# Kernel tuning notes

Measured on AMD Instinct MI355X. Metric: run time of the kernel, lower is better.

Reference implementation:

```python
import jax, jax.numpy as jnp
import numpy as np

B, C, H, W = 8, 512, 32, 32
NUM_HEADS = 8
NUM_GROUPS = 32
EPS = 1e-5


def setup_inputs() -> dict:
    key = jax.random.key(0)
    ks = jax.random.split(key, 7)
    x = jax.random.normal(ks[0], (B, C, H, W), dtype=jnp.float32)
    # GroupNorm affine params
    gamma = jnp.ones((C,), dtype=jnp.float32)
    beta = jnp.zeros((C,), dtype=jnp.float32)
    # qkv 1x1 conv1d: weight [3C, C], bias [3C]
    w_qkv = jax.random.normal(ks[1], (3 * C, C), dtype=jnp.float32) * (1.0 / np.sqrt(C))
    b_qkv = jax.random.normal(ks[2], (3 * C,), dtype=jnp.float32) * 0.01
    # proj_out 1x1 conv1d (zero-init in the original; random here so the op is non-trivial)
    w_proj = jax.random.normal(ks[3], (C, C), dtype=jnp.float32) * (1.0 / np.sqrt(C))
    b_proj = jax.random.normal(ks[4], (C,), dtype=jnp.float32) * 0.01
    return {"x": x, "gamma": gamma, "beta": beta, "w_qkv": w_qkv, "b_qkv": b_qkv,
            "w_proj": w_proj, "b_proj": b_proj}


def _group_norm(x, gamma, beta):
    # x: [B, C, L]
    b, c, l = x.shape
    xg = x.reshape(b, NUM_GROUPS, (c // NUM_GROUPS) * l)
    mean = jnp.mean(xg, axis=-1, keepdims=True)
    var = jnp.var(xg, axis=-1, keepdims=True)
    xn = ((xg - mean) * jax.lax.rsqrt(var + EPS)).reshape(b, c, l)
    return xn * gamma[None, :, None] + beta[None, :, None]


def reference(x, gamma, beta, w_qkv, b_qkv, w_proj, b_proj):
    b, c, h, w = x.shape
    L = h * w
    xf = x.reshape(b, c, L)
    xn = _group_norm(xf, gamma, beta)
    # 1x1 conv1d == channel matmul: [B, 3C, L]
    qkv = jnp.einsum('oc,bcl->bol', w_qkv, xn) + b_qkv[None, :, None]
    ch = c // NUM_HEADS  # per-head channels
    q, k, v = jnp.split(qkv, 3, axis=1)
    bh = b * NUM_HEADS
    q = q.reshape(bh, ch, L)
    k = k.reshape(bh, ch, L)
    v = v.reshape(bh, ch, L)
    scale = 1.0 / np.sqrt(np.sqrt(ch))
    weight = jnp.einsum('bct,bcs->bts', q * scale, k * scale)  # [BH, L, L]
    weight = jax.nn.softmax(weight.astype(jnp.float32), axis=-1).astype(q.dtype)
    a = jnp.einsum('bts,bcs->bct', weight, v)  # [BH, ch, L]
    hid = a.reshape(b, c, L)
    hid = jnp.einsum('oc,bcl->bol', w_proj, hid) + b_proj[None, :, None]
    return (xf + hid).reshape(b, c, h, w)
```

## Files before the change

kernel.cpp:

```cpp
#include <hip/hip_runtime.h>

typedef unsigned short u16;
using bf16x8 = __attribute__((ext_vector_type(8))) __bf16;
using f32x4  = __attribute__((ext_vector_type(4))) float;
using f32x16 = __attribute__((ext_vector_type(16))) float;
using u16x8  = __attribute__((ext_vector_type(8))) u16;
using u32x2  = __attribute__((ext_vector_type(2))) unsigned;

constexpr float QSC = 0.180336880111112f;

#define TID ((int)threadIdx.x)

__device__ __forceinline__ float fexp2(float x) {
#if __has_builtin(__builtin_amdgcn_exp2f)
  return __builtin_amdgcn_exp2f(x);
#else
  return exp2f(x);
#endif
}
__device__ __forceinline__ u16 f2bf(float f) {
  __bf16 h = (__bf16)f;
  return __builtin_bit_cast(u16, h);
}
__device__ __forceinline__ unsigned cvtpk(float a, float b) {
  unsigned r;
  asm("v_cvt_pk_bf16_f32 %0, %1, %2" : "=v"(r) : "v"(a), "v"(b));
  return r;
}
__device__ __forceinline__ u32x2 plswap(unsigned d, unsigned s) {
#if __has_builtin(__builtin_amdgcn_permlane32_swap)
  return __builtin_amdgcn_permlane32_swap(d, s, false, false);
#else
  unsigned dx = (unsigned)__shfl_xor((int)d, 32);
  unsigned sx = (unsigned)__shfl_xor((int)s, 32);
  int hh = ((int)threadIdx.x >> 5) & 1;
  u32x2 r;
  r[0] = hh ? d : sx;
  r[1] = hh ? dx : s;
  return r;
#endif
}
__device__ __forceinline__ float xhalf_max(float x) {
  unsigned u = __builtin_bit_cast(unsigned, x);
  u32x2 r = plswap(u, u);
  return fmaxf(__builtin_bit_cast(float, r[0]), __builtin_bit_cast(float, r[1]));
}
__device__ __forceinline__ float xhalf_add(float x) {
  unsigned u = __builtin_bit_cast(unsigned, x);
  u32x2 r = plswap(u, u);
  return __builtin_bit_cast(float, r[0]) + __builtin_bit_cast(float, r[1]);
}
__device__ __forceinline__ bf16x8 ldfrag(const u16* p) {
  return __builtin_bit_cast(bf16x8, *(const u16x8*)p);
}
__device__ __forceinline__ int swz(int row, int ch) {
  return ch ^ (row & 7) ^ ((row >> 3) & 7);
}
__device__ __forceinline__ void gload16(const u16* g, u16* l) {
  __builtin_amdgcn_global_load_lds(
      (__attribute__((address_space(1))) void*)g,
      (__attribute__((address_space(3))) void*)l, 16, 0, 0);
}
__device__ __forceinline__ f32x4 mfma16(bf16x8 a, bf16x8 b, f32x4 c) {
  return __builtin_amdgcn_mfma_f32_16x16x32_bf16(a, b, c, 0, 0, 0);
}
__device__ __forceinline__ f32x16 mfma32(bf16x8 a, bf16x8 b, f32x16 c) {
  return __builtin_amdgcn_mfma_f32_32x32x16_bf16(a, b, c, 0, 0, 0);
}

__global__ __launch_bounds__(256) void prep_stats(
    const float* __restrict__ wq, const float* __restrict__ wp,
    u16* __restrict__ wqb, u16* __restrict__ wpb,
    const float* __restrict__ x, float* __restrict__ stats) {
  __shared__ float sm[4], ssm[4];
  int bid = blockIdx.x;
  if (bid < 1024) {
    int i = bid * 256 + TID;
    if (i < 196608) {
      float4 v = ((const float4*)wq)[i];
      u16* o = wqb + i * 4;
      o[0] = f2bf(v.x); o[1] = f2bf(v.y); o[2] = f2bf(v.z); o[3] = f2bf(v.w);
    } else {
      int j = i - 196608;
      float4 v = ((const float4*)wp)[j];
      u16* o = wpb + j * 4;
      o[0] = f2bf(v.x); o[1] = f2bf(v.y); o[2] = f2bf(v.z); o[3] = f2bf(v.w);
    }
    return;
  }
  int blk = bid - 1024;
  size_t base = ((size_t)blk) << 14;
  const float4* xp = (const float4*)(x + base);
  float s = 0.f, ss = 0.f;
#pragma unroll
  for (int i = 0; i < 16; ++i) {
    float4 v = xp[TID + i * 256];
    s += v.x + v.y + v.z + v.w;
    ss += v.x * v.x + v.y * v.y + v.z * v.z + v.w * v.w;
  }
#pragma unroll
  for (int off = 32; off; off >>= 1) {
    s += __shfl_down(s, off);
    ss += __shfl_down(ss, off);
  }
  if ((TID & 63) == 0) { sm[TID >> 6] = s; ssm[TID >> 6] = ss; }
  __syncthreads();
  if (TID == 0) {
    float tot = sm[0] + sm[1] + sm[2] + sm[3];
    float tots = ssm[0] + ssm[1] + ssm[2] + ssm[3];
    float mean = tot * (1.f / 16384.f);
    float var = tots * (1.f / 16384.f) - mean * mean;
    stats[blk * 2] = mean;
    stats[blk * 2 + 1] = rsqrtf(var + 1e-5f);
  }
}

__global__ __launch_bounds__(256) void gn_apply(
    const float* __restrict__ x, const float* __restrict__ gamma,
    const float* __restrict__ beta, const float* __restrict__ stats,
    u16* __restrict__ xnT) {
  __shared__ u16 xt[32 * 520];
  int l0 = blockIdx.x * 32, b = blockIdx.y;
  int li = TID & 31, cb = TID >> 5;
#pragma unroll 4
  for (int it = 0; it < 64; ++it) {
    int c = it * 8 + cb;
    int g = c >> 4;
    float mean = stats[(b * 32 + g) * 2];
    float rstd = stats[(b * 32 + g) * 2 + 1];
    float ga = gamma[c] * rstd;
    float be = beta[c] - mean * ga;
    float v = x[((size_t)b * 512 + c) * 1024 + l0 + li];
    xt[li * 520 + c] = f2bf(v * ga + be);
  }
  __syncthreads();
  int li2 = TID >> 3, u0 = TID & 7;
#pragma unroll
  for (int it = 0; it < 8; ++it) {
    int unit = u0 + it * 8;
    u16x8 v = *(const u16x8*)&xt[li2 * 520 + unit * 8];
    *(u16x8*)&xnT[((size_t)b * 1024 + l0 + li2) * 512 + unit * 8] = v;
  }
}

__global__ __launch_bounds__(256) void qkv_gemm(
    const u16* __restrict__ A, const u16* __restrict__ Bt,
    const float* __restrict__ bias,
    u16* __restrict__ qT, u16* __restrict__ kT, u16* __restrict__ vbuf) {
  __shared__ u16 Al[8192], Bl[8192];
  int lin = blockIdx.x;
  int b = lin & 7;
  int rem = lin >> 3;
  int mi = rem % 12, ni = rem / 12;
  int m0 = mi * 128, n0 = ni * 128;
  int lane = TID & 63, w = TID >> 6;
  int mw = (w >> 1) * 64, nw = (w & 1) * 64;
  const u16* Bb = Bt + (size_t)b * 1024 * 512;
  f32x4 acc[4][4] = {};
  for (int k0 = 0; k0 < 512; k0 += 64) {
#pragma unroll
    for (int u = 0; u < 4; ++u) {
      int unit = u * 256 + TID, row = unit >> 3, ch = unit & 7;
      gload16(&A[(size_t)(m0 + row) * 512 + k0 + swz(row, ch) * 8], &Al[unit * 8]);
      gload16(&Bb[(size_t)(n0 + row) * 512 + k0 + swz(row, ch) * 8], &Bl[unit * 8]);
    }
    __syncthreads();
    bf16x8 xf[4][2];
#pragma unroll
    for (int xi = 0; xi < 4; ++xi)
#pragma unroll
      for (int kf = 0; kf < 2; ++kf) {
        int row = nw + xi * 16 + (lane & 15);
        int lc = kf * 4 + (lane >> 4);
        xf[xi][kf] = ldfrag(&Bl[row * 64 + swz(row, lc) * 8]);
      }
#pragma unroll
    for (int yi = 0; yi < 4; ++yi) {
      int row = mw + yi * 16 + (lane & 15);
      int lc = lane >> 4;
      bf16x8 y0 = ldfrag(&Al[row * 64 + swz(row, lc) * 8]);
      bf16x8 y1 = ldfrag(&Al[row * 64 + swz(row, lc + 4) * 8]);
#pragma unroll
      for (int xi = 0; xi < 4; ++xi) {
        acc[xi][yi] = mfma16(xf[xi][0], y0, acc[xi][yi]);
        acc[xi][yi] = mfma16(xf[xi][1], y1, acc[xi][yi]);
      }
    }
    __syncthreads();
  }
  int sel = m0 >> 9;
  int ho = w >> 1;
  u16* RP = ho ? Bl : Al;
  if (sel < 2) {
#pragma unroll
    for (int xi = 0; xi < 4; ++xi)
#pragma unroll
      for (int yi = 0; yi < 4; ++yi)
#pragma unroll
        for (int r = 0; r < 4; ++r) {
          int lloc = nw + xi * 16 + (lane >> 4) * 4 + r;
          int oc = yi * 16 + (lane & 15);
          float v = acc[xi][yi][r] + bias[m0 + ho * 64 + oc];
          if (sel == 0) v *= QSC;
          RP[lloc * 64 + swz(lloc, oc >> 3) * 8 + (oc & 7)] = f2bf(v);
        }
    __syncthreads();
    u16* dst = sel ? kT : qT;
    int h0 = (m0 & 511) >> 6;
#pragma unroll
    for (int uu = 0; uu < 4; ++uu) {
      int unit = uu * 256 + TID, row = unit >> 3, ch = unit & 7;
      u16x8 v0 = *(const u16x8*)&Al[row * 64 + swz(row, ch) * 8];
      u16x8 v1 = *(const u16x8*)&Bl[row * 64 + swz(row, ch) * 8];
      *(u16x8*)&dst[((size_t)(b * 8 + h0) * 1024 + n0 + row) * 64 + ch * 8] = v0;
      *(u16x8*)&dst[((size_t)(b * 8 + h0 + 1) * 1024 + n0 + row) * 64 + ch * 8] = v1;
    }
  } else {
#pragma unroll
    for (int xi = 0; xi < 4; ++xi)
#pragma unroll
      for (int yi = 0; yi < 4; ++yi)
#pragma unroll
        for (int r = 0; r < 4; ++r) {
          int lloc = nw + xi * 16 + (lane >> 4) * 4 + r;
          int oc = yi * 16 + (lane & 15);
          float v = acc[xi][yi][r] + bias[m0 + ho * 64 + oc];
          RP[oc * 128 + swz(oc, lloc >> 3) * 8 + (lloc & 7)] = f2bf(v);
        }
    __syncthreads();
    int h0 = (m0 - 1024) >> 6;
#pragma unroll
    for (int uu = 0; uu < 4; ++uu) {
      int unit = uu * 256 + TID, ro = unit >> 4, ch = unit & 15;
      u16x8 v0 = *(const u16x8*)&Al[ro * 128 + swz(ro, ch) * 8];
      u16x8 v1 = *(const u16x8*)&Bl[ro * 128 + swz(ro, ch) * 8];
      *(u16x8*)&vbuf[((size_t)(b * 8 + h0) * 64 + ro) * 1024 + n0 + ch * 8] = v0;
      *(u16x8*)&vbuf[((size_t)(b * 8 + h0 + 1) * 64 + ro) * 1024 + n0 + ch * 8] = v1;
    }
  }
}

__global__ __launch_bounds__(256) void attn_mfma(const u16* __restrict__ qT,
                                                 const u16* __restrict__ kT,
                                                 const u16* __restrict__ vb,
                                                 u16* __restrict__ aT) {
  __shared__ u16 smem[16384];
  int lin = blockIdx.x;
  int rem = lin >> 3;
  int bh = (lin & 7) * 8 + (rem >> 3);
  int t0 = (rem & 7) * 128;
  int b = bh >> 3, hd = bh & 7;
  int lane = TID & 63, w = TID >> 6;
  int h = lane >> 5, ln = lane & 31;
  int t = t0 + w * 32 + ln;
  const u16* qp = qT + ((size_t)bh * 1024 + t) * 64;
  const u16* kbase = kT + (size_t)bh * 1024 * 64;
  const u16* vbase = vb + (size_t)bh * 64 * 1024;
  bf16x8 qf[4];
#pragma unroll
  for (int kc = 0; kc < 4; ++kc) qf[kc] = ldfrag(qp + kc * 16 + h * 8);
  float m_r = -1e30f, l_r = 0.f;
  f32x16 oacc[2] = {};

  int u0 = TID, u1 = TID + 256;
  int r0 = u0 >> 3, c0 = u0 & 7;
  int r1 = u1 >> 3, c1 = u1 & 7;
  {
    u16* Ks = smem;
    u16* Vs = smem + 4096;
    gload16(&kbase[(size_t)r0 * 64 + swz(r0, c0) * 8], &Ks[u0 * 8]);
    gload16(&kbase[(size_t)r1 * 64 + swz(r1, c1) * 8], &Ks[u1 * 8]);
    gload16(&vbase[(size_t)r0 * 1024 + swz(r0, c0) * 8], &Vs[u0 * 8]);
    gload16(&vbase[(size_t)r1 * 1024 + swz(r1, c1) * 8], &Vs[u1 * 8]);
  }
  __syncthreads();
  for (int tile = 0; tile < 16; ++tile) {
    const u16* Ks = smem + (tile & 1) * 8192;
    const u16* Vs = Ks + 4096;
    if (tile < 15) {
      int sn = (tile + 1) * 64;
      u16* Kn = smem + ((tile + 1) & 1) * 8192;
      u16* Vn = Kn + 4096;
      gload16(&kbase[(size_t)(sn + r0) * 64 + swz(r0, c0) * 8], &Kn[u0 * 8]);
      gload16(&kbase[(size_t)(sn + r1) * 64 + swz(r1, c1) * 8], &Kn[u1 * 8]);
      gload16(&vbase[(size_t)r0 * 1024 + sn + swz(r0, c0) * 8], &Vn[u0 * 8]);
      gload16(&vbase[(size_t)r1 * 1024 + sn + swz(r1, c1) * 8], &Vn[u1 * 8]);
    }
    f32x16 sacc[2] = {};
    __builtin_amdgcn_s_setprio(1);
#pragma unroll
    for (int sb = 0; sb < 2; ++sb) {
      int srow = sb * 32 + ln;
#pragma unroll
      for (int kc = 0; kc < 4; ++kc) {
        bf16x8 kf = ldfrag(&Ks[srow * 64 + swz(srow, kc * 2 + h) * 8]);
        sacc[sb] = mfma32(kf, qf[kc], sacc[sb]);
      }
    }
    __builtin_amdgcn_s_setprio(0);
    float mp[4];
#pragma unroll
    for (int q = 0; q < 4; ++q) {
      mp[q] = fmaxf(fmaxf(sacc[0][q * 4], sacc[0][q * 4 + 1]),
                    fmaxf(sacc[0][q * 4 + 2], sacc[0][q * 4 + 3]));
      mp[q] = fmaxf(mp[q], fmaxf(fmaxf(sacc[1][q * 4], sacc[1][q * 4 + 1]),
                                 fmaxf(sacc[1][q * 4 + 2], sacc[1][q * 4 + 3])));
    }
    float mx = xhalf_max(fmaxf(fmaxf(mp[0], mp[1]), fmaxf(mp[2], mp[3])));
    bool noresc = (__all(mx <= m_r + 8.f) != 0);
    if (!noresc) {
      float mn = fmaxf(m_r, mx);
      float al = fexp2(m_r - mn);
      m_r = mn;
      l_r *= al;
#pragma unroll
      for (int ca = 0; ca < 2; ++ca)
#pragma unroll
        for (int i = 0; i < 16; ++i) oacc[ca][i] *= al;
    }
    float rp[4] = {0.f, 0.f, 0.f, 0.f};
#pragma unroll
    for (int sb = 0; sb < 2; ++sb)
#pragma unroll
      for (int i = 0; i < 16; ++i) {
        float pv = fexp2(sacc[sb][i] - m_r);
        sacc[sb][i] = pv;
        rp[i & 3] += pv;
      }
    l_r += xhalf_add((rp[0] + rp[1]) + (rp[2] + rp[3]));
    unsigned W[2][4][2];
#pragma unroll
    for (int sb = 0; sb < 2; ++sb)
#pragma unroll
      for (int p4 = 0; p4 < 4; ++p4)
#pragma unroll
        for (int e = 0; e < 2; ++e)
          W[sb][p4][e] = cvtpk(sacc[sb][p4 * 4 + 2 * e], sacc[sb][p4 * 4 + 2 * e + 1]);
#pragma unroll
    for (int m = 0; m < 4; ++m) {
      int sb = m >> 1, q = (m & 1) * 2;
      unsigned a0 = W[sb][q][0], a1 = W[sb][q][1];
      unsigned b0 = W[sb][q + 1][0], b1 = W[sb][q + 1][1];
      unsigned s0w = h ? a0 : b0;
      unsigned s1w = h ? a1 : b1;
      unsigned x0 = (unsigned)__shfl_xor((int)s0w, 32);
      unsigned x1 = (unsigned)__shfl_xor((int)s1w, 32);
      unsigned w0 = h ? x0 : a0;
      unsigned w1 = h ? x1 : a1;
      unsigned w2 = h ? b0 : x0;
      unsigned w3 = h ? b1 : x1;
      uint4 pw = make_uint4(w0, w1, w2, w3);
      bf16x8 pf = __builtin_bit_cast(bf16x8, pw);
      __builtin_amdgcn_s_setprio(1);
#pragma unroll
      for (int ca = 0; ca < 2; ++ca) {
        int crow = ca * 32 + ln;
        bf16x8 vf = ldfrag(&Vs[crow * 64 + swz(crow, m * 2 + h) * 8]);
        oacc[ca] = mfma32(vf, pf, oacc[ca]);
      }
      __builtin_amdgcn_s_setprio(0);
    }
    __syncthreads();
  }
  float rl = 1.f / l_r;
  int tloc = w * 32 + ln;
#pragma unroll
  for (int ca = 0; ca < 2; ++ca)
#pragma unroll
    for (int p4 = 0; p4 < 4; ++p4)
#pragma unroll
      for (int e = 0; e < 2; ++e) {
        int r = p4 * 4 + e * 2;
        int c = ca * 32 + 8 * p4 + 4 * h + 2 * e;
        unsigned pk = cvtpk(oacc[ca][r] * rl, oacc[ca][r + 1] * rl);
        *(unsigned*)&smem[tloc * 64 + swz(tloc, c >> 3) * 8 + (c & 7)] = pk;
      }
  __syncthreads();
#pragma unroll
  for (int u = 0; u < 4; ++u) {
    int unit = u * 256 + TID;
    int row = unit >> 3, ch = unit & 7;
    u16x8 v = *(const u16x8*)&smem[row * 64 + swz(row, ch) * 8];
    *(u16x8*)&aT[((size_t)b * 1024 + t0 + row) * 512 + hd * 64 + ch * 8] = v;
  }
}

__global__ __launch_bounds__(256) void proj_gemm(
    const u16* __restrict__ A, const u16* __restrict__ Bt,
    const float* __restrict__ bias, const float* __restrict__ resid,
    float* __restrict__ of) {
  __shared__ u16 Al[8192], Bl[8192];
  int lin = blockIdx.x;
  int b = lin & 7;
  int rem = lin >> 3;
  int mi = rem & 3, ni = rem >> 2;
  int m0 = mi * 128, n0 = ni * 128;
  int lane = TID & 63, w = TID >> 6;
  int mw = (w >> 1) * 64, nw = (w & 1) * 64;
  const u16* Bb = Bt + (size_t)b * 1024 * 512;
  f32x4 acc[4][4] = {};
  for (int k0 = 0; k0 < 512; k0 += 64) {
#pragma unroll
    for (int u = 0; u < 4; ++u) {
      int unit = u * 256 + TID, row = unit >> 3, ch = unit & 7;
      gload16(&A[(size_t)(m0 + row) * 512 + k0 + swz(row, ch) * 8], &Al[unit * 8]);
      gload16(&Bb[(size_t)(n0 + row) * 512 + k0 + swz(row, ch) * 8], &Bl[unit * 8]);
    }
    __syncthreads();
    bf16x8 xf[4][2];
#pragma unroll
    for (int xi = 0; xi < 4; ++xi)
#pragma unroll
      for (int kf = 0; kf < 2; ++kf) {
        int row = mw + xi * 16 + (lane & 15);
        int lc = kf * 4 + (lane >> 4);
        xf[xi][kf] = ldfrag(&Al[row * 64 + swz(row, lc) * 8]);
      }
#pragma unroll
    for (int yi = 0; yi < 4; ++yi) {
      int row = nw + yi * 16 + (lane & 15);
      int lc = lane >> 4;
      bf16x8 y0 = ldfrag(&Bl[row * 64 + swz(row, lc) * 8]);
      bf16x8 y1 = ldfrag(&Bl[row * 64 + swz(row, lc + 4) * 8]);
#pragma unroll
      for (int xi = 0; xi < 4; ++xi) {
        acc[xi][yi] = mfma16(xf[xi][0], y0, acc[xi][yi]);
        acc[xi][yi] = mfma16(xf[xi][1], y1, acc[xi][yi]);
      }
    }
    __syncthreads();
  }
#pragma unroll
  for (int xi = 0; xi < 4; ++xi)
#pragma unroll
    for (int yi = 0; yi < 4; ++yi)
#pragma unroll
      for (int r = 0; r < 4; ++r) {
        int o = m0 + mw + xi * 16 + (lane >> 4) * 4 + r;
        int l = n0 + nw + yi * 16 + (lane & 15);
        size_t idx = ((size_t)b * 512 + o) * 1024 + l;
        of[idx] = acc[xi][yi][r] + bias[o] + resid[idx];
      }
}

extern "C" void kernel_launch(void* const* d_in, const int* in_sizes, int n_in,
                              void* d_out, int out_size, void* d_ws, size_t ws_size,
                              hipStream_t stream) {
  const float* x = (const float*)d_in[0];
  const float* gamma = (const float*)d_in[1];
  const float* beta = (const float*)d_in[2];
  const float* w_qkv = (const float*)d_in[3];
  const float* b_qkv = (const float*)d_in[4];
  const float* w_proj = (const float*)d_in[5];
  const float* b_proj = (const float*)d_in[6];
  float* out = (float*)d_out;

  u16* qT = (u16*)d_ws;
  u16* kT = qT + 4194304;
  u16* vbuf = kT + 4194304;
  u16* aTb = vbuf + 4194304;
  u16* wqb = aTb + 4194304;
  u16* wpb = wqb + 786432;
  float* stats = (float*)(wpb + 262144);
  u16* xnT = (u16*)d_out;

  prep_stats<<<dim3(1280), dim3(256), 0, stream>>>(w_qkv, w_proj, wqb, wpb, x, stats);
  gn_apply<<<dim3(32, 8), dim3(256), 0, stream>>>(x, gamma, beta, stats, xnT);
  qkv_gemm<<<dim3(768), dim3(256), 0, stream>>>(wqb, xnT, b_qkv, qT, kT, vbuf);
  attn_mfma<<<dim3(512), dim3(256), 0, stream>>>(qT, kT, vbuf, aTb);
  proj_gemm<<<dim3(256), dim3(256), 0, stream>>>(wpb, aTb, b_proj, x, out);
}
```

Before: 87.34 us.

## Double KV stage size in attention and halve proj GEMM N-tile

The attention kernel now stages 128 keys and values per shared-memory buffer instead of 64, so it runs 8 outer iterations with two 64-wide sub-steps each. This halves the number of barriers and prefetch rounds, at the cost of doubling LDS to 64KB, which may lower occupancy. The projection GEMM uses 128x64 tiles with each wave computing a 32x64 slice, doubling the grid to 512 blocks to fill more CUs. This trades per-block data reuse for more parallelism.

Result: slower. 89.49 us (+2.5%).

```diff
diff --git a/kernel.cpp b/kernel.cpp
--- a/kernel.cpp
+++ b/kernel.cpp
@@ -244,7 +244,7 @@
                                                  const u16* __restrict__ kT,
                                                  const u16* __restrict__ vb,
                                                  u16* __restrict__ aT) {
-  __shared__ u16 smem[16384];
+  __shared__ u16 smem[32768];
   int lin = blockIdx.x;
   int rem = lin >> 3;
   int bh = (lin & 7) * 8 + (rem >> 3);
@@ -262,103 +262,121 @@
   float m_r = -1e30f, l_r = 0.f;
   f32x16 oacc[2] = {};
 
-  int u0 = TID, u1 = TID + 256;
-  int r0 = u0 >> 3, c0 = u0 & 7;
-  int r1 = u1 >> 3, c1 = u1 & 7;
   {
-    u16* Ks = smem;
-    u16* Vs = smem + 4096;
-    gload16(&kbase[(size_t)r0 * 64 + swz(r0, c0) * 8], &Ks[u0 * 8]);
-    gload16(&kbase[(size_t)r1 * 64 + swz(r1, c1) * 8], &Ks[u1 * 8]);
-    gload16(&vbase[(size_t)r0 * 1024 + swz(r0, c0) * 8], &Vs[u0 * 8]);
-    gload16(&vbase[(size_t)r1 * 1024 + swz(r1, c1) * 8], &Vs[u1 * 8]);
+    u16* Kb = smem;
+    u16* Vb = smem + 8192;
+#pragma unroll
+    for (int it = 0; it < 4; ++it) {
+      int unit = it * 256 + TID, row = unit >> 3, ch = unit & 7;
+      gload16(&kbase[(size_t)row * 64 + swz(row, ch) * 8], &Kb[unit * 8]);
+    }
+#pragma unroll
+    for (int it = 0; it < 4; ++it) {
+      int unit = it * 256 + TID;
+      int half = unit >> 9, c = (unit >> 3) & 63, ch = unit & 7;
+      gload16(&vbase[(size_t)c * 1024 + half * 64 + swz(c, ch) * 8], &Vb[unit * 8]);
+    }
   }
   __syncthreads();
-  for (int tile = 0; tile < 16; ++tile) {
-    const u16* Ks = smem + (tile & 1) * 8192;
-    const u16* Vs = Ks + 4096;
-    if (tile < 15) {
-      int sn = (tile + 1) * 64;
-      u16* Kn = smem + ((tile + 1) & 1) * 8192;
-      u16* Vn = Kn + 4096;
-      gload16(&kbase[(size_t)(sn + r0) * 64 + swz(r0, c0) * 8], &Kn[u0 * 8]);
-      gload16(&kbase[(size_t)(sn + r1) * 64 + swz(r1, c1) * 8], &Kn[u1 * 8]);
-      gload16(&vbase[(size_t)r0 * 1024 + sn + swz(r0, c0) * 8], &Vn[u0 * 8]);
-      gload16(&vbase[(size_t)r1 * 1024 + sn + swz(r1, c1) * 8], &Vn[u1 * 8]);
-    }
-    f32x16 sacc[2] = {};
-    __builtin_amdgcn_s_setprio(1);
-#pragma unroll
-    for (int sb = 0; sb < 2; ++sb) {
-      int srow = sb * 32 + ln;
-#pragma unroll
-      for (int kc = 0; kc < 4; ++kc) {
-        bf16x8 kf = ldfrag(&Ks[srow * 64 + swz(srow, kc * 2 + h) * 8]);
-        sacc[sb] = mfma32(kf, qf[kc], sacc[sb]);
-      }
-    }
-    __builtin_amdgcn_s_setprio(0);
-    float mp[4];
-#pragma unroll
-    for (int q = 0; q < 4; ++q) {
-      mp[q] = fmaxf(fmaxf(sacc[0][q * 4], sacc[0][q * 4 + 1]),
-                    fmaxf(sacc[0][q * 4 + 2], sacc[0][q * 4 + 3]));
-      mp[q] = fmaxf(mp[q], fmaxf(fmaxf(sacc[1][q * 4], sacc[1][q * 4 + 1]),
-                                 fmaxf(sacc[1][q * 4 + 2], sacc[1][q * 4 + 3])));
-    }
-    float mx = xhalf_max(fmaxf(fmaxf(mp[0], mp[1]), fmaxf(mp[2], mp[3])));
-    bool noresc = (__all(mx <= m_r + 8.f) != 0);
-    if (!noresc) {
-      float mn = fmaxf(m_r, mx);
-      float al = fexp2(m_r - mn);
-      m_r = mn;
-      l_r *= al;
-#pragma unroll
-      for (int ca = 0; ca < 2; ++ca)
-#pragma unroll
-        for (int i = 0; i < 16; ++i) oacc[ca][i] *= al;
-    }
-    float rp[4] = {0.f, 0.f, 0.f, 0.f};
-#pragma unroll
-    for (int sb = 0; sb < 2; ++sb)
-#pragma unroll
-      for (int i = 0; i < 16; ++i) {
-        float pv = fexp2(sacc[sb][i] - m_r);
-        sacc[sb][i] = pv;
-        rp[i & 3] += pv;
-      }
-    l_r += xhalf_add((rp[0] + rp[1]) + (rp[2] + rp[3]));
-    unsigned W[2][4][2];
-#pragma unroll
-    for (int sb = 0; sb < 2; ++sb)
-#pragma unroll
-      for (int p4 = 0; p4 < 4; ++p4)
-#pragma unroll
-        for (int e = 0; e < 2; ++e)
-          W[sb][p4][e] = cvtpk(sacc[sb][p4 * 4 + 2 * e], sacc[sb][p4 * 4 + 2 * e + 1]);
-#pragma unroll
-    for (int m = 0; m < 4; ++m) {
-      int sb = m >> 1, q = (m & 1) * 2;
-      unsigned a0 = W[sb][q][0], a1 = W[sb][q][1];
-      unsigned b0 = W[sb][q + 1][0], b1 = W[sb][q + 1][1];
-      unsigned s0w = h ? a0 : b0;
-      unsigned s1w = h ? a1 : b1;
-      unsigned x0 = (unsigned)__shfl_xor((int)s0w, 32);
-      unsigned x1 = (unsigned)__shfl_xor((int)s1w, 32);
-      unsigned w0 = h ? x0 : a0;
-      unsigned w1 = h ? x1 : a1;
-      unsigned w2 = h ? b0 : x0;
-      unsigned w3 = h ? b1 : x1;
-      uint4 pw = make_uint4(w0, w1, w2, w3);
-      bf16x8 pf = __builtin_bit_cast(bf16x8, pw);
+  for (int tile = 0; tile < 8; ++tile) {
+    const u16* Kb = smem + (tile & 1) * 16384;
+    const u16* Vb = Kb + 8192;
+    if (tile < 7) {
+      int sn = (tile + 1) * 128;
+      u16* Kn = smem + ((tile + 1) & 1) * 16384;
+      u16* Vn = Kn + 8192;
+#pragma unroll
+      for (int it = 0; it < 4; ++it) {
+        int unit = it * 256 + TID, row = unit >> 3, ch = unit & 7;
+        gload16(&kbase[(size_t)(sn + row) * 64 + swz(row, ch) * 8], &Kn[unit * 8]);
+      }
+#pragma unroll
+      for (int it = 0; it < 4; ++it) {
+        int unit = it * 256 + TID;
+        int half = unit >> 9, c = (unit >> 3) & 63, ch = unit & 7;
+        gload16(&vbase[(size_t)c * 1024 + sn + half * 64 + swz(c, ch) * 8],
+                &Vn[unit * 8]);
+      }
+    }
+#pragma unroll
+    for (int sub = 0; sub < 2; ++sub) {
+      const u16* Ks = Kb + sub * 4096;
+      const u16* Vs = Vb + sub * 4096;
+      f32x16 sacc[2] = {};
       __builtin_amdgcn_s_setprio(1);
 #pragma unroll
-      for (int ca = 0; ca < 2; ++ca) {
-        int crow = ca * 32 + ln;
-        bf16x8 vf = ldfrag(&Vs[crow * 64 + swz(crow, m * 2 + h) * 8]);
-        oacc[ca] = mfma32(vf, pf, oacc[ca]);
+      for (int sb = 0; sb < 2; ++sb) {
+        int srow = sb * 32 + ln;
+#pragma unroll
+        for (int kc = 0; kc < 4; ++kc) {
+          bf16x8 kf = ldfrag(&Ks[srow * 64 + swz(srow, kc * 2 + h) * 8]);
+          sacc[sb] = mfma32(kf, qf[kc], sacc[sb]);
+        }
       }
       __builtin_amdgcn_s_setprio(0);
+      float mp[4];
+#pragma unroll
+      for (int q = 0; q < 4; ++q) {
+        mp[q] = fmaxf(fmaxf(sacc[0][q * 4], sacc[0][q * 4 + 1]),
+                      fmaxf(sacc[0][q * 4 + 2], sacc[0][q * 4 + 3]));
+        mp[q] = fmaxf(mp[q], fmaxf(fmaxf(sacc[1][q * 4], sacc[1][q * 4 + 1]),
+                                   fmaxf(sacc[1][q * 4 + 2], sacc[1][q * 4 + 3])));
+      }
+      float mx = xhalf_max(fmaxf(fmaxf(mp[0], mp[1]), fmaxf(mp[2], mp[3])));
+      bool noresc = (__all(mx <= m_r + 8.f) != 0);
+      if (!noresc) {
+        float mn = fmaxf(m_r, mx);
+        float al = fexp2(m_r - mn);
+        m_r = mn;
+        l_r *= al;
+#pragma unroll
+        for (int ca = 0; ca < 2; ++ca)
+#pragma unroll
+          for (int i = 0; i < 16; ++i) oacc[ca][i] *= al;
+      }
+      float rp[4] = {0.f, 0.f, 0.f, 0.f};
+#pragma unroll
+      for (int sb = 0; sb < 2; ++sb)
+#pragma unroll
+        for (int i = 0; i < 16; ++i) {
+          float pv = fexp2(sacc[sb][i] - m_r);
+          sacc[sb][i] = pv;
+          rp[i & 3] += pv;
+        }
+      l_r += xhalf_add((rp[0] + rp[1]) + (rp[2] + rp[3]));
+      unsigned W[2][4][2];
+#pragma unroll
+      for (int sb = 0; sb < 2; ++sb)
+#pragma unroll
+        for (int p4 = 0; p4 < 4; ++p4)
+#pragma unroll
+          for (int e = 0; e < 2; ++e)
+            W[sb][p4][e] =
+                cvtpk(sacc[sb][p4 * 4 + 2 * e], sacc[sb][p4 * 4 + 2 * e + 1]);
+#pragma unroll
+      for (int m = 0; m < 4; ++m) {
+        int sb = m >> 1, q = (m & 1) * 2;
+        unsigned a0 = W[sb][q][0], a1 = W[sb][q][1];
+        unsigned b0 = W[sb][q + 1][0], b1 = W[sb][q + 1][1];
+        unsigned s0w = h ? a0 : b0;
+        unsigned s1w = h ? a1 : b1;
+        unsigned x0 = (unsigned)__shfl_xor((int)s0w, 32);
+        unsigned x1 = (unsigned)__shfl_xor((int)s1w, 32);
+        unsigned w0 = h ? x0 : a0;
+        unsigned w1 = h ? x1 : a1;
+        unsigned w2 = h ? b0 : x0;
+        unsigned w3 = h ? b1 : x1;
+        uint4 pw = make_uint4(w0, w1, w2, w3);
+        bf16x8 pf = __builtin_bit_cast(bf16x8, pw);
+        __builtin_amdgcn_s_setprio(1);
+#pragma unroll
+        for (int ca = 0; ca < 2; ++ca) {
+          int crow = ca * 32 + ln;
+          bf16x8 vf = ldfrag(&Vs[crow * 64 + swz(crow, m * 2 + h) * 8]);
+          oacc[ca] = mfma32(vf, pf, oacc[ca]);
+        }
+        __builtin_amdgcn_s_setprio(0);
+      }
     }
     __syncthreads();
   }
@@ -389,41 +407,45 @@
     const u16* __restrict__ A, const u16* __restrict__ Bt,
     const float* __restrict__ bias, const float* __restrict__ resid,
     float* __restrict__ of) {
-  __shared__ u16 Al[8192], Bl[8192];
+  __shared__ u16 Al[8192], Bl[4096];
   int lin = blockIdx.x;
   int b = lin & 7;
   int rem = lin >> 3;
-  int mi = rem & 3, ni = rem >> 2;
-  int m0 = mi * 128, n0 = ni * 128;
+  int mi = rem & 3, ni4 = rem >> 2;
+  int m0 = mi * 128, n0 = ni4 * 64;
   int lane = TID & 63, w = TID >> 6;
-  int mw = (w >> 1) * 64, nw = (w & 1) * 64;
+  int mw2 = w * 32;
   const u16* Bb = Bt + (size_t)b * 1024 * 512;
-  f32x4 acc[4][4] = {};
+  f32x4 acc[2][4] = {};
   for (int k0 = 0; k0 < 512; k0 += 64) {
 #pragma unroll
     for (int u = 0; u < 4; ++u) {
       int unit = u * 256 + TID, row = unit >> 3, ch = unit & 7;
       gload16(&A[(size_t)(m0 + row) * 512 + k0 + swz(row, ch) * 8], &Al[unit * 8]);
+    }
+#pragma unroll
+    for (int u = 0; u < 2; ++u) {
+      int unit = u * 256 + TID, row = unit >> 3, ch = unit & 7;
       gload16(&Bb[(size_t)(n0 + row) * 512 + k0 + swz(row, ch) * 8], &Bl[unit * 8]);
     }
     __syncthreads();
-    bf16x8 xf[4][2];
-#pragma unroll
-    for (int xi = 0; xi < 4; ++xi)
+    bf16x8 xf[2][2];
+#pragma unroll
+    for (int xi = 0; xi < 2; ++xi)
 #pragma unroll
       for (int kf = 0; kf < 2; ++kf) {
-        int row = mw + xi * 16 + (lane & 15);
+        int row = mw2 + xi * 16 + (lane & 15);
         int lc = kf * 4 + (lane >> 4);
         xf[xi][kf] = ldfrag(&Al[row * 64 + swz(row, lc) * 8]);
       }
 #pragma unroll
     for (int yi = 0; yi < 4; ++yi) {
-      int row = nw + yi * 16 + (lane & 15);
+      int row = yi * 16 + (lane & 15);
       int lc = lane >> 4;
       bf16x8 y0 = ldfrag(&Bl[row * 64 + swz(row, lc) * 8]);
       bf16x8 y1 = ldfrag(&Bl[row * 64 + swz(row, lc + 4) * 8]);
 #pragma unroll
-      for (int xi = 0; xi < 4; ++xi) {
+      for (int xi = 0; xi < 2; ++xi) {
         acc[xi][yi] = mfma16(xf[xi][0], y0, acc[xi][yi]);
         acc[xi][yi] = mfma16(xf[xi][1], y1, acc[xi][yi]);
       }
@@ -431,13 +453,13 @@
     __syncthreads();
   }
 #pragma unroll
-  for (int xi = 0; xi < 4; ++xi)
+  for (int xi = 0; xi < 2; ++xi)
 #pragma unroll
     for (int yi = 0; yi < 4; ++yi)
 #pragma unroll
       for (int r = 0; r < 4; ++r) {
-        int o = m0 + mw + xi * 16 + (lane >> 4) * 4 + r;
-        int l = n0 + nw + yi * 16 + (lane & 15);
+        int o = m0 + mw2 + xi * 16 + (lane >> 4) * 4 + r;
+        int l = n0 + yi * 16 + (lane & 15);
         size_t idx = ((size_t)b * 512 + o) * 1024 + l;
         of[idx] = acc[xi][yi][r] + bias[o] + resid[idx];
       }
@@ -468,5 +490,5 @@
   gn_apply<<<dim3(32, 8), dim3(256), 0, stream>>>(x, gamma, beta, stats, xnT);
   qkv_gemm<<<dim3(768), dim3(256), 0, stream>>>(wqb, xnT, b_qkv, qT, kT, vbuf);
   attn_mfma<<<dim3(512), dim3(256), 0, stream>>>(qT, kT, vbuf, aTb);
-  proj_gemm<<<dim3(256), dim3(256), 0, stream>>>(wpb, aTb, b_proj, x, out);
-}
+  proj_gemm<<<dim3(512), dim3(256), 0, stream>>>(wpb, aTb, b_proj, x, out);
+}
```

## Split attention KV sequence across two wave groups per block and merge softmax states

Applied to the files above, without the earlier changes.

The attention kernel now launches 512 threads per block, with two groups of four waves each processing half of the key/value sequence for the same 128 query rows. Each tile stage loads K/V for both halves into a larger double-buffered shared memory region, halving the loop trip count. At the end, the groups exchange running max and sum through shared memory, rescale their partial outputs, and group 0 combines them before normalizing and writing. This doubles wave-level parallelism per block to better hide latency, at the cost of double the shared memory (64KB) and extra merge traffic and barriers.

New measurement: 86.52 us, median of 3. No clear change (-0.9%).

```diff
diff --git a/kernel.cpp b/kernel.cpp
--- a/kernel.cpp
+++ b/kernel.cpp
@@ -240,19 +240,21 @@
   }
 }
 
-__global__ __launch_bounds__(256) void attn_mfma(const u16* __restrict__ qT,
+__global__ __launch_bounds__(512) void attn_mfma(const u16* __restrict__ qT,
                                                  const u16* __restrict__ kT,
                                                  const u16* __restrict__ vb,
                                                  u16* __restrict__ aT) {
-  __shared__ u16 smem[16384];
+  __shared__ u16 smem[32768];
   int lin = blockIdx.x;
   int rem = lin >> 3;
   int bh = (lin & 7) * 8 + (rem >> 3);
   int t0 = (rem & 7) * 128;
   int b = bh >> 3, hd = bh & 7;
-  int lane = TID & 63, w = TID >> 6;
+  int tid = TID;
+  int lane = tid & 63, w = tid >> 6;
+  int grp = w >> 2, qw = w & 3;
   int h = lane >> 5, ln = lane & 31;
-  int t = t0 + w * 32 + ln;
+  int t = t0 + qw * 32 + ln;
   const u16* qp = qT + ((size_t)bh * 1024 + t) * 64;
   const u16* kbase = kT + (size_t)bh * 1024 * 64;
   const u16* vbase = vb + (size_t)bh * 64 * 1024;
@@ -262,30 +264,30 @@
   float m_r = -1e30f, l_r = 0.f;
   f32x16 oacc[2] = {};
 
-  int u0 = TID, u1 = TID + 256;
-  int r0 = u0 >> 3, c0 = u0 & 7;
-  int r1 = u1 >> 3, c1 = u1 & 7;
-  {
-    u16* Ks = smem;
-    u16* Vs = smem + 4096;
-    gload16(&kbase[(size_t)r0 * 64 + swz(r0, c0) * 8], &Ks[u0 * 8]);
-    gload16(&kbase[(size_t)r1 * 64 + swz(r1, c1) * 8], &Ks[u1 * 8]);
-    gload16(&vbase[(size_t)r0 * 1024 + swz(r0, c0) * 8], &Vs[u0 * 8]);
-    gload16(&vbase[(size_t)r1 * 1024 + swz(r1, c1) * 8], &Vs[u1 * 8]);
-  }
+  auto STAGE = [&](int sn, u16* base) {
+#pragma unroll
+    for (int it = 0; it < 2; ++it) {
+      int unit = it * 512 + tid;
+      int g2 = unit >> 9, row = (unit >> 3) & 63, ch = unit & 7;
+      gload16(&kbase[(size_t)(g2 * 512 + sn + row) * 64 + swz(row, ch) * 8],
+              &base[unit * 8]);
+    }
+#pragma unroll
+    for (int it = 0; it < 2; ++it) {
+      int unit = it * 512 + tid;
+      int g2 = unit >> 9, c = (unit >> 3) & 63, ch = unit & 7;
+      gload16(&vbase[(size_t)c * 1024 + g2 * 512 + sn + swz(c, ch) * 8],
+              &base[8192 + unit * 8]);
+    }
+  };
+
+  STAGE(0, smem);
   __syncthreads();
-  for (int tile = 0; tile < 16; ++tile) {
-    const u16* Ks = smem + (tile & 1) * 8192;
-    const u16* Vs = Ks + 4096;
-    if (tile < 15) {
-      int sn = (tile + 1) * 64;
-      u16* Kn = smem + ((tile + 1) & 1) * 8192;
-      u16* Vn = Kn + 4096;
-      gload16(&kbase[(size_t)(sn + r0) * 64 + swz(r0, c0) * 8], &Kn[u0 * 8]);
-      gload16(&kbase[(size_t)(sn + r1) * 64 + swz(r1, c1) * 8], &Kn[u1 * 8]);
-      gload16(&vbase[(size_t)r0 * 1024 + sn + swz(r0, c0) * 8], &Vn[u0 * 8]);
-      gload16(&vbase[(size_t)r1 * 1024 + sn + swz(r1, c1) * 8], &Vn[u1 * 8]);
-    }
+  for (int tile = 0; tile < 8; ++tile) {
+    u16* base = smem + (tile & 1) * 16384;
+    const u16* Ks = base + grp * 4096;
+    const u16* Vs = base + 8192 + grp * 4096;
+    if (tile < 7) STAGE((tile + 1) * 64, smem + ((tile + 1) & 1) * 16384);
     f32x16 sacc[2] = {};
     __builtin_amdgcn_s_setprio(1);
 #pragma unroll
@@ -362,23 +364,51 @@
     }
     __syncthreads();
   }
-  float rl = 1.f / l_r;
-  int tloc = w * 32 + ln;
+  float* mlb = (float*)(smem + 8192);
+  float* obuf = (float*)(smem + 16384);
+  int slot = qw * 64 + lane;
+  mlb[(grp * 256 + slot) * 2 + 0] = m_r;
+  mlb[(grp * 256 + slot) * 2 + 1] = l_r;
+  __syncthreads();
+  float m2 = mlb[((grp ^ 1) * 256 + slot) * 2 + 0];
+  float l2 = mlb[((grp ^ 1) * 256 + slot) * 2 + 1];
+  float mm = fmaxf(m_r, m2);
+  float aown = fexp2(m_r - mm);
+  float lm = l_r * aown + l2 * fexp2(m2 - mm);
 #pragma unroll
   for (int ca = 0; ca < 2; ++ca)
 #pragma unroll
-    for (int p4 = 0; p4 < 4; ++p4)
-#pragma unroll
-      for (int e = 0; e < 2; ++e) {
-        int r = p4 * 4 + e * 2;
-        int c = ca * 32 + 8 * p4 + 4 * h + 2 * e;
-        unsigned pk = cvtpk(oacc[ca][r] * rl, oacc[ca][r + 1] * rl);
-        *(unsigned*)&smem[tloc * 64 + swz(tloc, c >> 3) * 8 + (c & 7)] = pk;
-      }
+    for (int i = 0; i < 16; ++i) oacc[ca][i] *= aown;
+  if (grp == 1) {
+#pragma unroll
+    for (int ca = 0; ca < 2; ++ca)
+#pragma unroll
+      for (int i = 0; i < 16; ++i) obuf[(ca * 16 + i) * 256 + slot] = oacc[ca][i];
+  }
   __syncthreads();
-#pragma unroll
-  for (int u = 0; u < 4; ++u) {
-    int unit = u * 256 + TID;
+  if (grp == 0) {
+#pragma unroll
+    for (int ca = 0; ca < 2; ++ca)
+#pragma unroll
+      for (int i = 0; i < 16; ++i) oacc[ca][i] += obuf[(ca * 16 + i) * 256 + slot];
+    float rl = 1.f / lm;
+    int tloc = qw * 32 + ln;
+#pragma unroll
+    for (int ca = 0; ca < 2; ++ca)
+#pragma unroll
+      for (int p4 = 0; p4 < 4; ++p4)
+#pragma unroll
+        for (int e = 0; e < 2; ++e) {
+          int r = p4 * 4 + e * 2;
+          int c = ca * 32 + 8 * p4 + 4 * h + 2 * e;
+          unsigned pk = cvtpk(oacc[ca][r] * rl, oacc[ca][r + 1] * rl);
+          *(unsigned*)&smem[tloc * 64 + swz(tloc, c >> 3) * 8 + (c & 7)] = pk;
+        }
+  }
+  __syncthreads();
+#pragma unroll
+  for (int u = 0; u < 2; ++u) {
+    int unit = u * 512 + tid;
     int row = unit >> 3, ch = unit & 7;
     u16x8 v = *(const u16x8*)&smem[row * 64 + swz(row, ch) * 8];
     *(u16x8*)&aT[((size_t)b * 1024 + t0 + row) * 512 + hd * 64 + ch * 8] = v;
@@ -467,6 +497,6 @@
   prep_stats<<<dim3(1280), dim3(256), 0, stream>>>(w_qkv, w_proj, wqb, wpb, x, stats);
   gn_apply<<<dim3(32, 8), dim3(256), 0, stream>>>(x, gamma, beta, stats, xnT);
   qkv_gemm<<<dim3(768), dim3(256), 0, stream>>>(wqb, xnT, b_qkv, qT, kT, vbuf);
-  attn_mfma<<<dim3(512), dim3(256), 0, stream>>>(qT, kT, vbuf, aTb);
+  attn_mfma<<<dim3(512), dim3(512), 0, stream>>>(qT, kT, vbuf, aTb);
   proj_gemm<<<dim3(256), dim3(256), 0, stream>>>(wpb, aTb, b_proj, x, out);
 }
```
